# Kernel optimization log

Measured on AMD Instinct MI355X. Metric: run time of the kernel, lower is better.

Reference implementation:

```python
import jax, jax.numpy as jnp
import numpy as np

B, NPG, F, DEG = 512, 512, 255, 32   # graphs, nodes-per-graph, feat dim, avg degree
N = B * NPG
E = N * DEG
RATIO = 0.5
K = int(np.ceil(RATIO * NPG))        # nodes kept per graph (static)


def setup_inputs() -> dict:
    key = jax.random.key(0)
    k1, k2, k3, k4, k5 = jax.random.split(key, 5)
    out = jax.random.normal(k1, (N, F), jnp.float32)
    z = jax.random.randint(k2, (N,), 0, 101)  # z == 100 marks virtual nodes
    # random edges strictly within each graph (block-contiguous node ids)
    local = jax.random.randint(k3, (2, B, NPG * DEG), 0, NPG)
    offs = (jnp.arange(B) * NPG)[None, :, None]
    edge_index = (local + offs).reshape(2, E)
    batch = jnp.repeat(jnp.arange(B), NPG)
    W = jax.random.normal(k4, (F + 1, 1), jnp.float32) * (1.0 / np.sqrt(F + 1))
    b = jnp.zeros((1,), jnp.float32)
    edge_attr = jax.random.normal(k5, (E, 1), jnp.float32)  # carried but unused by SAGPool scoring
    return dict(out=out, z=z, edge_index=edge_index, batch=batch, W=W, b=b,
                edge_attr=edge_attr)


def gcn_score(x, edge_index, W, b):
    """GCNConv(F+1 -> 1) with self-loops and symmetric normalization."""
    n = x.shape[0]
    h = (x @ W)[:, 0]  # [N] since out_channels == 1
    row, col = edge_index[0], edge_index[1]
    loop = jnp.arange(n)
    row = jnp.concatenate([row, loop])
    col = jnp.concatenate([col, loop])
    deg = jax.ops.segment_sum(jnp.ones_like(col, x.dtype), col, num_segments=n)
    dinv = jnp.where(deg > 0, jax.lax.rsqrt(deg), 0.0)
    norm = dinv[row] * dinv[col]  # deg^-1/2 * deg^-1/2 per edge
    agg = jax.ops.segment_sum(norm * h[row], col, num_segments=n)
    return agg + b[0]


def reference(out, z, edge_index, batch, W, b, edge_attr):
    # concat real/virtual bit
    real = (z != 100).astype(out.dtype)[:, None]
    x = jnp.concatenate([out, real], axis=-1)          # [N, F+1]
    # SAGPooling: score nodes, tanh nonlinearity
    score = jnp.tanh(gcn_score(x, edge_index, W, b))   # [N]
    # per-graph top-k (uniform graph size -> static-shape top_k)
    sv, si = jax.lax.top_k(score.reshape(B, NPG), K)   # [B, K]
    perm = (si + (jnp.arange(B) * NPG)[:, None]).reshape(-1)  # global node ids
    xp = x[perm] * sv.reshape(-1)[:, None]             # gated selected nodes [B*K, F+1]
    # global_mean_pool over pooled batch (k nodes per graph)
    return xp.reshape(B, K, F + 1).mean(axis=1)        # [B, F+1]
```

## Files before the change

kernel.cpp:

```cpp
#include <hip/hip_runtime.h>
#include <math.h>

#define NPG     512
#define B_GR    512
#define FDIM    255
#define DEG     32
#define EPG     (NPG * DEG)
#define N_NODES (B_GR * NPG)
#define E_TOT   (N_NODES * DEG)
#define K_KEEP  256

__global__ __launch_bounds__(1024, 8) void k_fused(const float* __restrict__ feat,
                                                   const int*   __restrict__ z,
                                                   const int*   __restrict__ ei,
                                                   const float* __restrict__ W,
                                                   const float* __restrict__ bias,
                                                   float*       __restrict__ outp) {
    __shared__ ushort4 cc4[EPG / 4];
    __shared__ __align__(16) float Wx[1020];
    __shared__ __align__(16) float score[NPG];
    __shared__ __align__(16) float v_l[NPG];
    __shared__ float dinv_l[NPG];
    __shared__ float agg[NPG];
    __shared__ float realb[NPG];
    __shared__ int   deg[NPG];
    __shared__ int   rank2[2][NPG];
    __shared__ int   selidx[K_KEEP];
    __shared__ float selsc[K_KEEP];
    __shared__ float red[3][256];
    __shared__ float w255s;
    __shared__ int   cnt;

    const int g     = blockIdx.x;
    const int tid   = threadIdx.x;
    const int nbase = g * NPG;
    const int lane  = tid & 63;
    const int wave  = tid >> 6;

    const int4* colp4 = (const int4*)(ei + (size_t)E_TOT + (size_t)g * EPG);
    const int4* rowp4 = (const int4*)(ei + (size_t)g * EPG);

    if (tid < 1020) Wx[tid] = W[tid % 255];
    if (tid == 0) { w255s = W[255]; cnt = 0; }
    if (tid < NPG) {
        realb[tid] = (z[nbase + tid] != 100) ? 1.f : 0.f;
        deg[tid]   = 1;
    }
    __syncthreads();

    {
        const bool l63 = (lane == 63);
        const float4 zero = make_float4(0.f, 0.f, 0.f, 0.f);
        const float4* W4 = (const float4*)Wx;
        const float4 wf0 = W4[lane];
        const float4 wf1 = W4[64 + lane];
        const float4 wf2 = W4[128 + lane];
        const float4 wf3 = l63 ? zero : W4[192 + lane];
        const float  w255 = w255s;
        const float4* F4 = (const float4*)(feat + (size_t)nbase * FDIM);
        float4* v4 = (float4*)v_l;

        for (int k = 0; k < 8; ++k) {
            const int grp = wave + (k << 4);
            const float4* src = F4 + (size_t)grp * 255;
            const float4 a = src[lane];
            const float4 b = src[64 + lane];
            const float4 c = src[128 + lane];
            const float4 d = l63 ? zero : src[192 + lane];

            float acc0 = a.x * wf0.x + a.y * wf0.y + a.z * wf0.z;
            const float p03 = a.w * wf0.w;
            float acc1 = b.x * wf1.x + b.y * wf1.y;
            const float p12 = b.z * wf1.z, p13 = b.w * wf1.w;
            float acc2 = c.x * wf2.x;
            const float p21 = c.y * wf2.y, p22 = c.z * wf2.z, p23 = c.w * wf2.w;
            float acc3 = d.x * wf3.x + d.y * wf3.y + d.z * wf3.z + d.w * wf3.w;

            const float q03 = p03;
            const float q1  = p12 + p13;
            const float q2  = p21 + p22 + p23;
            acc0 += l63 ? 0.f : q03;
            acc1 += l63 ? q03 : q1;
            acc2 += l63 ? q1  : q2;
            acc3 += l63 ? q2  : 0.f;

#pragma unroll
            for (int off = 32; off; off >>= 1) {
                acc0 += __shfl_down(acc0, off, 64);
                acc1 += __shfl_down(acc1, off, 64);
                acc2 += __shfl_down(acc2, off, 64);
                acc3 += __shfl_down(acc3, off, 64);
            }
            if (lane == 0) {
                const int n0 = grp * 4;
                float4 hv;
                hv.x = acc0 + realb[n0 + 0] * w255;
                hv.y = acc1 + realb[n0 + 1] * w255;
                hv.z = acc2 + realb[n0 + 2] * w255;
                hv.w = acc3 + realb[n0 + 3] * w255;
                v4[grp] = hv;
            }
        }
    }
    __syncthreads();

    {
        int4 c4v[4], r4v[4];
#pragma unroll
        for (int it = 0; it < 4; ++it) c4v[it] = colp4[it * 1024 + tid];
#pragma unroll
        for (int it = 0; it < 4; ++it) r4v[it] = rowp4[it * 1024 + tid];

#pragma unroll
        for (int it = 0; it < 4; ++it) {
            const int4 c4 = c4v[it];
            ushort4 u;
            u.x = (unsigned short)(c4.x - nbase);
            u.y = (unsigned short)(c4.y - nbase);
            u.z = (unsigned short)(c4.z - nbase);
            u.w = (unsigned short)(c4.w - nbase);
            cc4[it * 1024 + tid] = u;
            atomicAdd(&deg[u.x], 1);
            atomicAdd(&deg[u.y], 1);
            atomicAdd(&deg[u.z], 1);
            atomicAdd(&deg[u.w], 1);
        }
        __syncthreads();

        if (tid < NPG) {
            const float di = (float)(1.0 / sqrt((double)deg[tid]));
            dinv_l[tid] = di;
            const float v = di * v_l[tid];
            v_l[tid] = v;
            agg[tid] = v;
        }
        __syncthreads();

#pragma unroll
        for (int it = 0; it < 4; ++it) {
            const ushort4 u  = cc4[it * 1024 + tid];
            const int4    r4 = r4v[it];
            atomicAdd(&agg[u.x], v_l[r4.x - nbase]);
            atomicAdd(&agg[u.y], v_l[r4.y - nbase]);
            atomicAdd(&agg[u.z], v_l[r4.z - nbase]);
            atomicAdd(&agg[u.w], v_l[r4.w - nbase]);
        }
        __syncthreads();
    }

    if (tid < NPG)
        score[tid] = tanhf(fmaf(agg[tid], dinv_l[tid], bias[0]));
    __syncthreads();

    {
        const int     node = tid & (NPG - 1);
        const int     half = tid >> 9;
        const float   sc   = score[node];
        const float4* s4p  = (const float4*)&score[half * 256];
        int part = 0;
#pragma unroll 8
        for (int i = 0; i < 64; ++i) {
            const float4 s4 = s4p[i];
            const int    j  = half * 256 + i * 4;
            part += (s4.x > sc) || (s4.x == sc && (j + 0) < node);
            part += (s4.y > sc) || (s4.y == sc && (j + 1) < node);
            part += (s4.z > sc) || (s4.z == sc && (j + 2) < node);
            part += (s4.w > sc) || (s4.w == sc && (j + 3) < node);
        }
        rank2[half][node] = part;
    }
    __syncthreads();

    if (tid < NPG) {
        const int rank = rank2[0][tid] + rank2[1][tid];
        if (rank < K_KEEP) {
            const int slot = atomicAdd(&cnt, 1);
            selidx[slot] = tid;
            selsc[slot]  = score[tid];
        }
    }
    __syncthreads();

    {
        const int f = tid & 255;
        const int q = tid >> 8;
        float acc = 0.f;
        if (f < FDIM) {
            const float* fb = feat + (size_t)nbase * FDIM + f;
#pragma unroll
            for (int k = 0; k < 64; k += 8) {
                int   is[8]; float ss[8]; float tv[8];
#pragma unroll
                for (int j = 0; j < 8; ++j) {
                    is[j] = selidx[q + 4 * (k + j)];
                    ss[j] = selsc [q + 4 * (k + j)];
                }
#pragma unroll
                for (int j = 0; j < 8; ++j)
                    tv[j] = fb[(size_t)is[j] * FDIM];
#pragma unroll
                for (int j = 0; j < 8; ++j)
                    acc = fmaf(ss[j], tv[j], acc);
            }
        } else {
            for (int s = q; s < K_KEEP; s += 4)
                acc = fmaf(selsc[s], realb[selidx[s]], acc);
        }
        if (q) red[q - 1][f] = acc;
        __syncthreads();
        if (q == 0)
            outp[(size_t)g * 256 + f] =
                (acc + red[0][f] + red[1][f] + red[2][f]) * (1.f / K_KEEP);
    }
}

extern "C" void kernel_launch(void* const* d_in, const int* in_sizes, int n_in,
                              void* d_out, int out_size, void* d_ws, size_t ws_size,
                              hipStream_t stream) {
    const float* feat = (const float*)d_in[0];
    const int*   z    = (const int*)  d_in[1];
    const int*   ei   = (const int*)  d_in[2];
    const float* W    = (const float*)d_in[4];
    const float* bias = (const float*)d_in[5];
    float* outp = (float*)d_out;

    k_fused<<<B_GR, 1024, 0, stream>>>(feat, z, ei, W, bias, outp);
}
```

Measured before the change: 131.1 us.

## Process two graphs per block, overlapping second projection with first graph's scoring

```diff
diff --git a/kernel.cpp b/kernel.cpp
--- a/kernel.cpp
+++ b/kernel.cpp
@@ -10,7 +10,7 @@
 #define E_TOT   (N_NODES * DEG)
 #define K_KEEP  256
 
-__global__ __launch_bounds__(1024, 8) void k_fused(const float* __restrict__ feat,
+__global__ __launch_bounds__(1024, 4) void k_fused(const float* __restrict__ feat,
                                                    const int*   __restrict__ z,
                                                    const int*   __restrict__ ei,
                                                    const float* __restrict__ W,
@@ -19,10 +19,12 @@
     __shared__ ushort4 cc4[EPG / 4];
     __shared__ __align__(16) float Wx[1020];
     __shared__ __align__(16) float score[NPG];
-    __shared__ __align__(16) float v_l[NPG];
+    __shared__ __align__(16) float v1[NPG];
+    __shared__ __align__(16) float v2[NPG];
     __shared__ float dinv_l[NPG];
     __shared__ float agg[NPG];
-    __shared__ float realb[NPG];
+    __shared__ float realb1[NPG];
+    __shared__ float realb2[NPG];
     __shared__ int   deg[NPG];
     __shared__ int   rank2[2][NPG];
     __shared__ int   selidx[K_KEEP];
@@ -31,94 +33,210 @@
     __shared__ float w255s;
     __shared__ int   cnt;
 
-    const int g     = blockIdx.x;
-    const int tid   = threadIdx.x;
-    const int nbase = g * NPG;
-    const int lane  = tid & 63;
-    const int wave  = tid >> 6;
-
-    const int4* colp4 = (const int4*)(ei + (size_t)E_TOT + (size_t)g * EPG);
-    const int4* rowp4 = (const int4*)(ei + (size_t)g * EPG);
+    const int b    = blockIdx.x;
+    const int g1   = 2 * b, g2 = 2 * b + 1;
+    const int tid  = threadIdx.x;
+    const int lane = tid & 63;
+    const int wave = tid >> 6;
+    const int nb1  = g1 * NPG, nb2 = g2 * NPG;
 
     if (tid < 1020) Wx[tid] = W[tid % 255];
-    if (tid == 0) { w255s = W[255]; cnt = 0; }
+    if (tid == 0) w255s = W[255];
     if (tid < NPG) {
-        realb[tid] = (z[nbase + tid] != 100) ? 1.f : 0.f;
-        deg[tid]   = 1;
-    }
-    __syncthreads();
-
-    {
-        const bool l63 = (lane == 63);
-        const float4 zero = make_float4(0.f, 0.f, 0.f, 0.f);
-        const float4* W4 = (const float4*)Wx;
-        const float4 wf0 = W4[lane];
-        const float4 wf1 = W4[64 + lane];
-        const float4 wf2 = W4[128 + lane];
-        const float4 wf3 = l63 ? zero : W4[192 + lane];
-        const float  w255 = w255s;
-        const float4* F4 = (const float4*)(feat + (size_t)nbase * FDIM);
-        float4* v4 = (float4*)v_l;
-
-        for (int k = 0; k < 8; ++k) {
-            const int grp = wave + (k << 4);
-            const float4* src = F4 + (size_t)grp * 255;
-            const float4 a = src[lane];
-            const float4 b = src[64 + lane];
-            const float4 c = src[128 + lane];
-            const float4 d = l63 ? zero : src[192 + lane];
-
-            float acc0 = a.x * wf0.x + a.y * wf0.y + a.z * wf0.z;
-            const float p03 = a.w * wf0.w;
-            float acc1 = b.x * wf1.x + b.y * wf1.y;
-            const float p12 = b.z * wf1.z, p13 = b.w * wf1.w;
-            float acc2 = c.x * wf2.x;
-            const float p21 = c.y * wf2.y, p22 = c.z * wf2.z, p23 = c.w * wf2.w;
-            float acc3 = d.x * wf3.x + d.y * wf3.y + d.z * wf3.z + d.w * wf3.w;
-
-            const float q03 = p03;
-            const float q1  = p12 + p13;
-            const float q2  = p21 + p22 + p23;
-            acc0 += l63 ? 0.f : q03;
-            acc1 += l63 ? q03 : q1;
-            acc2 += l63 ? q1  : q2;
-            acc3 += l63 ? q2  : 0.f;
-
-#pragma unroll
-            for (int off = 32; off; off >>= 1) {
-                acc0 += __shfl_down(acc0, off, 64);
-                acc1 += __shfl_down(acc1, off, 64);
-                acc2 += __shfl_down(acc2, off, 64);
-                acc3 += __shfl_down(acc3, off, 64);
+        realb1[tid] = (z[nb1 + tid] != 100) ? 1.f : 0.f;
+        deg[tid]    = 1;
+    } else {
+        realb2[tid - NPG] = (z[nb2 + tid - NPG] != 100) ? 1.f : 0.f;
+    }
+    __syncthreads();
+
+    const bool   l63   = (lane == 63);
+    const float4 zero4 = make_float4(0.f, 0.f, 0.f, 0.f);
+    const float4* W4   = (const float4*)Wx;
+    const float4 wf0 = W4[lane];
+    const float4 wf1 = W4[64 + lane];
+    const float4 wf2 = W4[128 + lane];
+    const float4 wf3 = l63 ? zero4 : W4[192 + lane];
+    const float  w255 = w255s;
+    const float  bb0  = bias[0];
+
+    auto proj_group = [&](const float4* F4, const float* rb, float4* vout, int grp) {
+        const float4* src = F4 + (size_t)grp * 255;
+        const float4 a = src[lane];
+        const float4 bq = src[64 + lane];
+        const float4 c = src[128 + lane];
+        const float4 d = l63 ? zero4 : src[192 + lane];
+
+        float acc0 = a.x * wf0.x + a.y * wf0.y + a.z * wf0.z;
+        const float p03 = a.w * wf0.w;
+        float acc1 = bq.x * wf1.x + bq.y * wf1.y;
+        const float p12 = bq.z * wf1.z, p13 = bq.w * wf1.w;
+        float acc2 = c.x * wf2.x;
+        const float p21 = c.y * wf2.y, p22 = c.z * wf2.z, p23 = c.w * wf2.w;
+        float acc3 = d.x * wf3.x + d.y * wf3.y + d.z * wf3.z + d.w * wf3.w;
+
+        const float q1 = p12 + p13;
+        const float q2 = p21 + p22 + p23;
+        acc0 += l63 ? 0.f : p03;
+        acc1 += l63 ? p03 : q1;
+        acc2 += l63 ? q1  : q2;
+        acc3 += l63 ? q2  : 0.f;
+
+#pragma unroll
+        for (int off = 32; off; off >>= 1) {
+            acc0 += __shfl_down(acc0, off, 64);
+            acc1 += __shfl_down(acc1, off, 64);
+            acc2 += __shfl_down(acc2, off, 64);
+            acc3 += __shfl_down(acc3, off, 64);
+        }
+        if (lane == 0) {
+            const int n0 = grp * 4;
+            float4 hv;
+            hv.x = acc0 + rb[n0 + 0] * w255;
+            hv.y = acc1 + rb[n0 + 1] * w255;
+            hv.z = acc2 + rb[n0 + 2] * w255;
+            hv.w = acc3 + rb[n0 + 3] * w255;
+            vout[grp] = hv;
+        }
+    };
+
+    {
+        const float4* F4 = (const float4*)(feat + (size_t)nb1 * FDIM);
+        float4* vo = (float4*)v1;
+        for (int k = 0; k < 8; ++k)
+            proj_group(F4, realb1, vo, wave + (k << 4));
+    }
+    __syncthreads();
+
+    const int4* colp1 = (const int4*)(ei + (size_t)E_TOT + (size_t)g1 * EPG);
+    const int4* rowp1 = (const int4*)(ei + (size_t)g1 * EPG);
+
+    for (int r = 0; r < 8; ++r) {
+        if (wave < 8) {
+            switch (r) {
+            case 0: case 1: {
+                for (int it = r * 4; it < r * 4 + 4; ++it) {
+                    const int  idx = it * 512 + tid;
+                    const int4 c4  = colp1[idx];
+                    ushort4 u;
+                    u.x = (unsigned short)(c4.x - nb1);
+                    u.y = (unsigned short)(c4.y - nb1);
+                    u.z = (unsigned short)(c4.z - nb1);
+                    u.w = (unsigned short)(c4.w - nb1);
+                    cc4[idx] = u;
+                    atomicAdd(&deg[u.x], 1);
+                    atomicAdd(&deg[u.y], 1);
+                    atomicAdd(&deg[u.z], 1);
+                    atomicAdd(&deg[u.w], 1);
+                }
+            } break;
+            case 2: {
+                const float di = (float)(1.0 / sqrt((double)deg[tid]));
+                dinv_l[tid] = di;
+                const float v = di * v1[tid];
+                v1[tid] = v;
+                agg[tid] = v;
+                if (tid == 0) cnt = 0;
+            } break;
+            case 3: case 4: {
+                for (int it = (r - 3) * 4; it < (r - 3) * 4 + 4; ++it) {
+                    const int     idx = it * 512 + tid;
+                    const int4    r4  = rowp1[idx];
+                    const ushort4 u   = cc4[idx];
+                    atomicAdd(&agg[u.x], v1[r4.x - nb1]);
+                    atomicAdd(&agg[u.y], v1[r4.y - nb1]);
+                    atomicAdd(&agg[u.z], v1[r4.z - nb1]);
+                    atomicAdd(&agg[u.w], v1[r4.w - nb1]);
+                }
+            } break;
+            case 5:
+                score[tid] = tanhf(fmaf(agg[tid], dinv_l[tid], bb0));
+                break;
+            case 6: {
+                const float   sc  = score[tid];
+                const float4* s4p = (const float4*)score;
+                int part = 0;
+                for (int i = 0; i < 128; ++i) {
+                    const float4 s4 = s4p[i];
+                    const int    j  = i * 4;
+                    part += (s4.x > sc) || (s4.x == sc && (j + 0) < tid);
+                    part += (s4.y > sc) || (s4.y == sc && (j + 1) < tid);
+                    part += (s4.z > sc) || (s4.z == sc && (j + 2) < tid);
+                    part += (s4.w > sc) || (s4.w == sc && (j + 3) < tid);
+                }
+                deg[tid] = part;
+            } break;
+            case 7: {
+                if (deg[tid] < K_KEEP) {
+                    const int slot = atomicAdd(&cnt, 1);
+                    selidx[slot] = tid;
+                    selsc[slot]  = score[tid];
+                }
+            } break;
             }
-            if (lane == 0) {
-                const int n0 = grp * 4;
-                float4 hv;
-                hv.x = acc0 + realb[n0 + 0] * w255;
-                hv.y = acc1 + realb[n0 + 1] * w255;
-                hv.z = acc2 + realb[n0 + 2] * w255;
-                hv.w = acc3 + realb[n0 + 3] * w255;
-                v4[grp] = hv;
+        } else {
+            const float4* F4 = (const float4*)(feat + (size_t)nb2 * FDIM);
+            float4* vo = (float4*)v2;
+            const int w16 = (wave - 8) * 16;
+            proj_group(F4, realb2, vo, w16 + 2 * r);
+            proj_group(F4, realb2, vo, w16 + 2 * r + 1);
+        }
+        __syncthreads();
+    }
+
+    {
+        const int f = tid & 255;
+        const int q = tid >> 8;
+        float acc = 0.f;
+        if (f < FDIM) {
+            const float* fb = feat + (size_t)nb1 * FDIM + f;
+#pragma unroll
+            for (int k = 0; k < 64; k += 8) {
+                int   is[8]; float ss[8]; float tv[8];
+#pragma unroll
+                for (int j = 0; j < 8; ++j) {
+                    is[j] = selidx[q + 4 * (k + j)];
+                    ss[j] = selsc [q + 4 * (k + j)];
+                }
+#pragma unroll
+                for (int j = 0; j < 8; ++j)
+                    tv[j] = fb[(size_t)is[j] * FDIM];
+#pragma unroll
+                for (int j = 0; j < 8; ++j)
+                    acc = fmaf(ss[j], tv[j], acc);
             }
-        }
-    }
-    __syncthreads();
+        } else {
+            for (int s = q; s < K_KEEP; s += 4)
+                acc = fmaf(selsc[s], realb1[selidx[s]], acc);
+        }
+        if (q) red[q - 1][f] = acc;
+        if (tid < NPG) deg[tid] = 1;
+        if (tid == 0)  cnt = 0;
+        __syncthreads();
+        if (q == 0)
+            outp[(size_t)g1 * 256 + f] =
+                (acc + red[0][f] + red[1][f] + red[2][f]) * (1.f / K_KEEP);
+    }
+    __syncthreads();
+
+    const int4* colp2 = (const int4*)(ei + (size_t)E_TOT + (size_t)g2 * EPG);
+    const int4* rowp2 = (const int4*)(ei + (size_t)g2 * EPG);
 
     {
         int4 c4v[4], r4v[4];
 #pragma unroll
-        for (int it = 0; it < 4; ++it) c4v[it] = colp4[it * 1024 + tid];
-#pragma unroll
-        for (int it = 0; it < 4; ++it) r4v[it] = rowp4[it * 1024 + tid];
+        for (int it = 0; it < 4; ++it) c4v[it] = colp2[it * 1024 + tid];
+#pragma unroll
+        for (int it = 0; it < 4; ++it) r4v[it] = rowp2[it * 1024 + tid];
 
 #pragma unroll
         for (int it = 0; it < 4; ++it) {
             const int4 c4 = c4v[it];
             ushort4 u;
-            u.x = (unsigned short)(c4.x - nbase);
-            u.y = (unsigned short)(c4.y - nbase);
-            u.z = (unsigned short)(c4.z - nbase);
-            u.w = (unsigned short)(c4.w - nbase);
+            u.x = (unsigned short)(c4.x - nb2);
+            u.y = (unsigned short)(c4.y - nb2);
+            u.z = (unsigned short)(c4.z - nb2);
+            u.w = (unsigned short)(c4.w - nb2);
             cc4[it * 1024 + tid] = u;
             atomicAdd(&deg[u.x], 1);
             atomicAdd(&deg[u.y], 1);
@@ -130,8 +248,8 @@
         if (tid < NPG) {
             const float di = (float)(1.0 / sqrt((double)deg[tid]));
             dinv_l[tid] = di;
-            const float v = di * v_l[tid];
-            v_l[tid] = v;
+            const float v = di * v2[tid];
+            v2[tid] = v;
             agg[tid] = v;
         }
         __syncthreads();
@@ -140,16 +258,16 @@
         for (int it = 0; it < 4; ++it) {
             const ushort4 u  = cc4[it * 1024 + tid];
             const int4    r4 = r4v[it];
-            atomicAdd(&agg[u.x], v_l[r4.x - nbase]);
-            atomicAdd(&agg[u.y], v_l[r4.y - nbase]);
-            atomicAdd(&agg[u.z], v_l[r4.z - nbase]);
-            atomicAdd(&agg[u.w], v_l[r4.w - nbase]);
+            atomicAdd(&agg[u.x], v2[r4.x - nb2]);
+            atomicAdd(&agg[u.y], v2[r4.y - nb2]);
+            atomicAdd(&agg[u.z], v2[r4.z - nb2]);
+            atomicAdd(&agg[u.w], v2[r4.w - nb2]);
         }
         __syncthreads();
     }
 
     if (tid < NPG)
-        score[tid] = tanhf(fmaf(agg[tid], dinv_l[tid], bias[0]));
+        score[tid] = tanhf(fmaf(agg[tid], dinv_l[tid], bb0));
     __syncthreads();
 
     {
@@ -186,7 +304,7 @@
         const int q = tid >> 8;
         float acc = 0.f;
         if (f < FDIM) {
-            const float* fb = feat + (size_t)nbase * FDIM + f;
+            const float* fb = feat + (size_t)nb2 * FDIM + f;
 #pragma unroll
             for (int k = 0; k < 64; k += 8) {
                 int   is[8]; float ss[8]; float tv[8];
@@ -204,12 +322,12 @@
             }
         } else {
             for (int s = q; s < K_KEEP; s += 4)
-                acc = fmaf(selsc[s], realb[selidx[s]], acc);
+                acc = fmaf(selsc[s], realb2[selidx[s]], acc);
         }
         if (q) red[q - 1][f] = acc;
         __syncthreads();
         if (q == 0)
-            outp[(size_t)g * 256 + f] =
+            outp[(size_t)g2 * 256 + f] =
                 (acc + red[0][f] + red[1][f] + red[2][f]) * (1.f / K_KEEP);
     }
 }
@@ -224,5 +342,5 @@
     const float* bias = (const float*)d_in[5];
     float* outp = (float*)d_out;
 
-    k_fused<<<B_GR, 1024, 0, stream>>>(feat, z, ei, W, bias, outp);
+    k_fused<<<B_GR / 2, 1024, 0, stream>>>(feat, z, ei, W, bias, outp);
 }
```

Measured after the change: 144.5 us. 10.2% more time.
